# Optimization experiments

Measured on AMD Instinct MI355X. Metric: run time of the kernel, lower is better.

Reference implementation:

```python
import jax, jax.numpy as jnp
import numpy as np
from jax import lax

T, B, I, H = 512, 256, 128, 256

def setup_inputs() -> dict:
    key = jax.random.key(0)
    k1, k2, k3, k4 = jax.random.split(key, 4)
    x = jax.random.normal(k1, (T, B, I), dtype=jnp.float32)
    h0 = jnp.zeros((B, H), dtype=jnp.float32)
    Wi = jax.random.normal(k2, (H, I), dtype=jnp.float32) * (1.0 / np.sqrt(I))
    Wh = jax.random.normal(k3, (H, H), dtype=jnp.float32) * (1.0 / np.sqrt(H))
    bh = jax.random.normal(k4, (H,), dtype=jnp.float32) * 0.01
    return {"x": x, "h0": h0, "Wi": Wi, "Wh": Wh, "bh": bh}

def reference(x, h0, Wi, Wh, bh):
    # Precompute input projection for all timesteps: [T, B, H]
    xi = jnp.einsum("tbi,hi->tbh", x, Wi) + bh
    def step(h, xi_t):
        h_new = jnp.tanh(xi_t + h @ Wh.T)
        return h_new, h_new
    _, hs = lax.scan(step, h0, xi)
    return hs  # [T, B, H] hidden states, matching torch stack(out[1:])
```

## Files before the change

kernel.cpp:

```cpp
#include <hip/hip_runtime.h>
#include <hip/hip_bf16.h>
#include <math.h>

#define TT 512
#define BB 256
#define II 128
#define HH 256

#define TANH_S 2.885390043258667f


#define FCHUNK(CNT, A0,A1,B0,B1,C0,C1,D0,D1, H0,H1) \
        "s_waitcnt lgkmcnt(" CNT ")\n" \
        "v_pk_fma_f32 v[32:33], v[" A0 "], v[" H0 "], v[32:33]\n" \
        "v_pk_fma_f32 v[34:35], v[" B0 "], v[" H0 "], v[34:35]\n" \
        "v_pk_fma_f32 v[36:37], v[" C0 "], v[" H0 "], v[36:37]\n" \
        "v_pk_fma_f32 v[38:39], v[" D0 "], v[" H0 "], v[38:39]\n" \
        "v_pk_fma_f32 v[32:33], v[" A1 "], v[" H1 "], v[32:33]\n" \
        "v_pk_fma_f32 v[34:35], v[" B1 "], v[" H1 "], v[34:35]\n" \
        "v_pk_fma_f32 v[36:37], v[" C1 "], v[" H1 "], v[36:37]\n" \
        "v_pk_fma_f32 v[38:39], v[" D1 "], v[" H1 "], v[38:39]\n"

#define HSTORE \
        "global_store_dword v25, v30, %[iob]\n" \
        "v_add_u32 v25, 0x40000, v25\n"

#define FBODY(XNR, XCR, VC, ST) \
        ST \
         \
        "s_and_saveexec_b64 s[86:87], %[mskx]\n" \
        "global_load_dwordx4 " XNR ", v18, %[xb]\n" \
        "s_mov_b64 exec, s[86:87]\n" \
        "v_add_u32 v18, 0x20000, v18\n" \
        "v_min_u32 v18, %[vxomax], v18\n" \
         \
        "ds_read_b128 v[40:43], v16\n" \
        "ds_read_b128 v[44:47], v16 offset:16\n" \
        "ds_read_b128 v[48:51], v16 offset:32\n" \
        "ds_read_b128 v[52:55], v16 offset:48\n" \
        "ds_read_b128 v[56:59], v16 offset:64\n" \
        "ds_read_b128 v[60:63], v16 offset:80\n" \
        "s_setprio 1\n" \
         \
        "s_waitcnt lgkmcnt(5)\n" \
        "v_pk_mul_f32 v[32:33], v[64:65],   v[40:41]\n" \
        "v_pk_mul_f32 v[34:35], v[96:97],   v[40:41]\n" \
        "v_pk_mul_f32 v[36:37], v[128:129], v[40:41]\n" \
        "v_pk_mul_f32 v[38:39], v[160:161], v[40:41]\n" \
        "v_pk_fma_f32 v[32:33], v[66:67],   v[42:43], v[32:33]\n" \
        "v_pk_fma_f32 v[34:35], v[98:99],   v[42:43], v[34:35]\n" \
        "v_pk_fma_f32 v[36:37], v[130:131], v[42:43], v[36:37]\n" \
        "v_pk_fma_f32 v[38:39], v[162:163], v[42:43], v[38:39]\n" \
        "ds_read_b128 v[40:43], v16 offset:96\n" \
        FCHUNK("5","68:69","70:71","100:101","102:103","132:133","134:135","164:165","166:167","44:45","46:47") \
        "ds_read_b128 v[44:47], v16 offset:112\n" \
        FCHUNK("5","72:73","74:75","104:105","106:107","136:137","138:139","168:169","170:171","48:49","50:51") \
        "ds_read_b128 v[48:51], v16 offset:128\n" \
        FCHUNK("5","76:77","78:79","108:109","110:111","140:141","142:143","172:173","174:175","52:53","54:55") \
        "ds_read_b128 v[52:55], v16 offset:144\n" \
        FCHUNK("5","80:81","82:83","112:113","114:115","144:145","146:147","176:177","178:179","56:57","58:59") \
        "ds_read_b128 v[56:59], v16 offset:160\n" \
        FCHUNK("5","84:85","86:87","116:117","118:119","148:149","150:151","180:181","182:183","60:61","62:63") \
        "ds_read_b128 v[60:63], v16 offset:176\n" \
        FCHUNK("5","88:89","90:91","120:121","122:123","152:153","154:155","184:185","186:187","40:41","42:43") \
        FCHUNK("4","92:93","94:95","124:125","126:127","156:157","158:159","188:189","190:191","44:45","46:47") \
        FCHUNK("3","192:193","194:195","208:209","210:211","224:225","226:227","240:241","242:243","48:49","50:51") \
        FCHUNK("2","196:197","198:199","212:213","214:215","228:229","230:231","244:245","246:247","52:53","54:55") \
        FCHUNK("1","200:201","202:203","216:217","218:219","232:233","234:235","248:249","250:251","56:57","58:59") \
        FCHUNK("0","204:205","206:207","220:221","222:223","236:237","238:239","252:253","254:255","60:61","62:63") \
        "s_setprio 0\n" \
         \
        "s_waitcnt vmcnt(" VC ")\n" \
        "s_and_saveexec_b64 s[86:87], %[mskx]\n" \
        "ds_write_b128 v24, " XCR "\n" \
        "s_mov_b64 exec, s[86:87]\n" \
        "v_xor_b32 v24, 0x800, v24\n" \
         \
        "v_add_f32 v32, v32, v33\n" \
        "v_add_f32 v34, v34, v35\n" \
        "v_add_f32 v36, v36, v37\n" \
        "v_add_f32 v38, v38, v39\n" \
         \
        "v_add_f32 v32, v32, v32 quad_perm:[1,0,3,2] row_mask:0xf bank_mask:0xf\n" \
        "v_add_f32 v34, v34, v34 quad_perm:[1,0,3,2] row_mask:0xf bank_mask:0xf\n" \
        "v_add_f32 v36, v36, v36 quad_perm:[1,0,3,2] row_mask:0xf bank_mask:0xf\n" \
        "v_add_f32 v38, v38, v38 quad_perm:[1,0,3,2] row_mask:0xf bank_mask:0xf\n" \
        "v_add_f32 v32, v32, v32 quad_perm:[2,3,0,1] row_mask:0xf bank_mask:0xf\n" \
        "v_add_f32 v34, v34, v34 quad_perm:[2,3,0,1] row_mask:0xf bank_mask:0xf\n" \
        "v_add_f32 v36, v36, v36 quad_perm:[2,3,0,1] row_mask:0xf bank_mask:0xf\n" \
        "v_add_f32 v38, v38, v38 quad_perm:[2,3,0,1] row_mask:0xf bank_mask:0xf\n" \
         \
        "v_cndmask_b32 v30, v32, v34, %[m0]\n" \
        "v_cndmask_b32 v31, v36, v38, %[m0]\n" \
        "v_cndmask_b32 v30, v30, v31, %[m1]\n" \
         \
        "s_nop 1\n" \
        "v_add_f32 v30, v30, v30 row_ror:8 row_mask:0xf bank_mask:0xf\n" \
         \
        "v_add_f32 v30, v30, v19\n" \
        "v_exp_f32 v31, v30\n" \
        "s_nop 0\n" \
        "v_add_f32 v31, 1.0, v31\n" \
        "v_rcp_f32 v31, v31\n" \
        "s_nop 0\n" \
        "v_fma_f32 v30, -2.0, v31, 1.0\n" \
         \
        "s_and_saveexec_b64 s[84:85], %[msk]\n" \
        "ds_write_b32 v17, v30\n" \
        "s_mov_b64 exec, s[84:85]\n" \
        "v_xor_b32 v17, 0x800, v17\n" \
        "s_waitcnt lgkmcnt(0)\n" \
        "s_barrier\n" \
        "v_xor_b32 v16, 0x800, v16\n"

#define SCALE_PAIR(P) "v_pk_mul_f32 v[" P "], v[" P "], v[26:27]\n"

__global__ __launch_bounds__(512, 2) void rnn_fused_kernel(
    const float* __restrict__ x,  const float* __restrict__ h0,
    const float* __restrict__ Wi, const float* __restrict__ Wh,
    const float* __restrict__ bh, float* __restrict__ out)
{
    __shared__ float hbuf[928];

    const int tid  = threadIdx.x;
    const int b    = blockIdx.x;
    const int lane = tid & 63;
    const int q    = tid >> 6;
    const int kg   = (lane & 3) | ((lane >> 1) & 4);
    const int cg   = ((lane >> 2) & 1) | ((lane >> 3) & 6);
    const int col0 = 32 * q + 4 * cg;
    const int col  = col0 + (kg & 3);

    const float* wp  = Wh + (size_t)col0 * HH + kg * 32;
    const float* wip = Wi + (size_t)col0 * II + kg * 16;
    const float* iob = out + (size_t)b * HH;
    const float* xb  = x   + (size_t)b * II;
    unsigned hbase = (unsigned)(size_t)&hbuf[0];
    unsigned hvr = hbase + kg * 208;
    unsigned hvw = hbase + 0x800 + q * 208 + (4 * cg + (kg & 3)) * 4;
    unsigned vxw = hbase + 0x800 + (tid >> 2) * 208 + 128 + 16 * (tid & 3);
    unsigned vxo = (unsigned)(16 * tid) + 0x20000u;
    unsigned vxomax = (unsigned)(16 * tid) + 511u * 0x20000u;
    unsigned vho = (unsigned)(col * 4);
    float bhv = bh[col] * TANH_S;
    unsigned long long m0   = __ballot((lane & 1) != 0);
    unsigned long long m1   = __ballot((lane & 2) != 0);
    unsigned long long msk  = __ballot(kg < 4);
    unsigned long long mskx = __ballot(tid < 32);

    if (tid < HH) hbuf[(tid >> 5) * 52 + (tid & 31)] = h0[(size_t)b * HH + tid];
    if (tid < II) hbuf[(tid >> 4) * 52 + 32 + (tid & 15)] = xb[tid];
    __syncthreads();

    asm volatile(
        "global_load_dwordx4 v[64:67],   %[wp], off\n"
        "global_load_dwordx4 v[68:71],   %[wp], off offset:16\n"
        "global_load_dwordx4 v[72:75],   %[wp], off offset:32\n"
        "global_load_dwordx4 v[76:79],   %[wp], off offset:48\n"
        "global_load_dwordx4 v[80:83],   %[wp], off offset:64\n"
        "global_load_dwordx4 v[84:87],   %[wp], off offset:80\n"
        "global_load_dwordx4 v[88:91],   %[wp], off offset:96\n"
        "global_load_dwordx4 v[92:95],   %[wp], off offset:112\n"
        "global_load_dwordx4 v[96:99],   %[wp], off offset:1024\n"
        "global_load_dwordx4 v[100:103], %[wp], off offset:1040\n"
        "global_load_dwordx4 v[104:107], %[wp], off offset:1056\n"
        "global_load_dwordx4 v[108:111], %[wp], off offset:1072\n"
        "global_load_dwordx4 v[112:115], %[wp], off offset:1088\n"
        "global_load_dwordx4 v[116:119], %[wp], off offset:1104\n"
        "global_load_dwordx4 v[120:123], %[wp], off offset:1120\n"
        "global_load_dwordx4 v[124:127], %[wp], off offset:1136\n"
        "global_load_dwordx4 v[128:131], %[wp], off offset:2048\n"
        "global_load_dwordx4 v[132:135], %[wp], off offset:2064\n"
        "global_load_dwordx4 v[136:139], %[wp], off offset:2080\n"
        "global_load_dwordx4 v[140:143], %[wp], off offset:2096\n"
        "global_load_dwordx4 v[144:147], %[wp], off offset:2112\n"
        "global_load_dwordx4 v[148:151], %[wp], off offset:2128\n"
        "global_load_dwordx4 v[152:155], %[wp], off offset:2144\n"
        "global_load_dwordx4 v[156:159], %[wp], off offset:2160\n"
        "global_load_dwordx4 v[160:163], %[wp], off offset:3072\n"
        "global_load_dwordx4 v[164:167], %[wp], off offset:3088\n"
        "global_load_dwordx4 v[168:171], %[wp], off offset:3104\n"
        "global_load_dwordx4 v[172:175], %[wp], off offset:3120\n"
        "global_load_dwordx4 v[176:179], %[wp], off offset:3136\n"
        "global_load_dwordx4 v[180:183], %[wp], off offset:3152\n"
        "global_load_dwordx4 v[184:187], %[wp], off offset:3168\n"
        "global_load_dwordx4 v[188:191], %[wp], off offset:3184\n"
        "global_load_dwordx4 v[192:195], %[wip], off\n"
        "global_load_dwordx4 v[196:199], %[wip], off offset:16\n"
        "global_load_dwordx4 v[200:203], %[wip], off offset:32\n"
        "global_load_dwordx4 v[204:207], %[wip], off offset:48\n"
        "global_load_dwordx4 v[208:211], %[wip], off offset:512\n"
        "global_load_dwordx4 v[212:215], %[wip], off offset:528\n"
        "global_load_dwordx4 v[216:219], %[wip], off offset:544\n"
        "global_load_dwordx4 v[220:223], %[wip], off offset:560\n"
        "global_load_dwordx4 v[224:227], %[wip], off offset:1024\n"
        "global_load_dwordx4 v[228:231], %[wip], off offset:1040\n"
        "global_load_dwordx4 v[232:235], %[wip], off offset:1056\n"
        "global_load_dwordx4 v[236:239], %[wip], off offset:1072\n"
        "global_load_dwordx4 v[240:243], %[wip], off offset:1536\n"
        "global_load_dwordx4 v[244:247], %[wip], off offset:1552\n"
        "global_load_dwordx4 v[248:251], %[wip], off offset:1568\n"
        "global_load_dwordx4 v[252:255], %[wip], off offset:1584\n"
        "v_mov_b32 v16, %[hvr]\n"
        "v_mov_b32 v17, %[hvw]\n"
        "v_mov_b32 v18, %[vxo]\n"
        "v_mov_b32 v19, %[bhv]\n"
        "v_mov_b32 v24, %[vxw]\n"
        "v_mov_b32 v25, %[vho]\n"
        "s_waitcnt vmcnt(0)\n"
        "v_mov_b32 v26, 0x4038aa3b\n"
        "v_mov_b32 v27, 0x4038aa3b\n"
        SCALE_PAIR("64:65")   SCALE_PAIR("66:67")   SCALE_PAIR("68:69")   SCALE_PAIR("70:71")
        SCALE_PAIR("72:73")   SCALE_PAIR("74:75")   SCALE_PAIR("76:77")   SCALE_PAIR("78:79")
        SCALE_PAIR("80:81")   SCALE_PAIR("82:83")   SCALE_PAIR("84:85")   SCALE_PAIR("86:87")
        SCALE_PAIR("88:89")   SCALE_PAIR("90:91")   SCALE_PAIR("92:93")   SCALE_PAIR("94:95")
        SCALE_PAIR("96:97")   SCALE_PAIR("98:99")   SCALE_PAIR("100:101") SCALE_PAIR("102:103")
        SCALE_PAIR("104:105") SCALE_PAIR("106:107") SCALE_PAIR("108:109") SCALE_PAIR("110:111")
        SCALE_PAIR("112:113") SCALE_PAIR("114:115") SCALE_PAIR("116:117") SCALE_PAIR("118:119")
        SCALE_PAIR("120:121") SCALE_PAIR("122:123") SCALE_PAIR("124:125") SCALE_PAIR("126:127")
        SCALE_PAIR("128:129") SCALE_PAIR("130:131") SCALE_PAIR("132:133") SCALE_PAIR("134:135")
        SCALE_PAIR("136:137") SCALE_PAIR("138:139") SCALE_PAIR("140:141") SCALE_PAIR("142:143")
        SCALE_PAIR("144:145") SCALE_PAIR("146:147") SCALE_PAIR("148:149") SCALE_PAIR("150:151")
        SCALE_PAIR("152:153") SCALE_PAIR("154:155") SCALE_PAIR("156:157") SCALE_PAIR("158:159")
        SCALE_PAIR("160:161") SCALE_PAIR("162:163") SCALE_PAIR("164:165") SCALE_PAIR("166:167")
        SCALE_PAIR("168:169") SCALE_PAIR("170:171") SCALE_PAIR("172:173") SCALE_PAIR("174:175")
        SCALE_PAIR("176:177") SCALE_PAIR("178:179") SCALE_PAIR("180:181") SCALE_PAIR("182:183")
        SCALE_PAIR("184:185") SCALE_PAIR("186:187") SCALE_PAIR("188:189") SCALE_PAIR("190:191")
        SCALE_PAIR("192:193") SCALE_PAIR("194:195") SCALE_PAIR("196:197") SCALE_PAIR("198:199")
        SCALE_PAIR("200:201") SCALE_PAIR("202:203") SCALE_PAIR("204:205") SCALE_PAIR("206:207")
        SCALE_PAIR("208:209") SCALE_PAIR("210:211") SCALE_PAIR("212:213") SCALE_PAIR("214:215")
        SCALE_PAIR("216:217") SCALE_PAIR("218:219") SCALE_PAIR("220:221") SCALE_PAIR("222:223")
        SCALE_PAIR("224:225") SCALE_PAIR("226:227") SCALE_PAIR("228:229") SCALE_PAIR("230:231")
        SCALE_PAIR("232:233") SCALE_PAIR("234:235") SCALE_PAIR("236:237") SCALE_PAIR("238:239")
        SCALE_PAIR("240:241") SCALE_PAIR("242:243") SCALE_PAIR("244:245") SCALE_PAIR("246:247")
        SCALE_PAIR("248:249") SCALE_PAIR("250:251") SCALE_PAIR("252:253") SCALE_PAIR("254:255")
        "s_and_saveexec_b64 s[86:87], %[mskx]\n"
        "global_load_dwordx4 v[26:29], v18, %[xb]\n"
        "s_mov_b64 exec, s[86:87]\n"
        "v_add_u32 v18, 0x20000, v18\n"
        "s_movk_i32 s82, 0xFF\n"
        FBODY("v[20:23]", "v[26:29]", "1", "")
        FBODY("v[26:29]", "v[20:23]", "2", HSTORE)
        "LTOP_%=:\n"
        FBODY("v[20:23]", "v[26:29]", "2", HSTORE)
        FBODY("v[26:29]", "v[20:23]", "2", HSTORE)
        "s_sub_u32 s82, s82, 1\n"
        "s_cmp_lg_u32 s82, 0\n"
        "s_cbranch_scc1 LTOP_%=\n"
        "global_store_dword v25, v30, %[iob]\n"
        :
        : [wp] "v"(wp), [wip] "v"(wip), [iob] "s"(iob), [xb] "s"(xb),
          [hvr] "v"(hvr), [hvw] "v"(hvw), [vxo] "v"(vxo),
          [vxomax] "v"(vxomax), [vxw] "v"(vxw), [vho] "v"(vho),
          [bhv] "v"(bhv),
          [m0] "s"(m0), [m1] "s"(m1), [msk] "s"(msk), [mskx] "s"(mskx)
        : "memory", "scc", "s82", "s84", "s85", "s86", "s87",
          "v16","v17","v18","v19","v20","v21","v22","v23",
          "v24","v25","v26","v27","v28","v29","v30","v31",
          "v32","v33","v34","v35","v36","v37","v38","v39",
          "v40","v41","v42","v43","v44","v45","v46","v47",
          "v48","v49","v50","v51","v52","v53","v54","v55",
          "v56","v57","v58","v59","v60","v61","v62","v63",
          "v64","v65","v66","v67","v68","v69","v70","v71",
          "v72","v73","v74","v75","v76","v77","v78","v79",
          "v80","v81","v82","v83","v84","v85","v86","v87",
          "v88","v89","v90","v91","v92","v93","v94","v95",
          "v96","v97","v98","v99","v100","v101","v102","v103",
          "v104","v105","v106","v107","v108","v109","v110","v111",
          "v112","v113","v114","v115","v116","v117","v118","v119",
          "v120","v121","v122","v123","v124","v125","v126","v127",
          "v128","v129","v130","v131","v132","v133","v134","v135",
          "v136","v137","v138","v139","v140","v141","v142","v143",
          "v144","v145","v146","v147","v148","v149","v150","v151",
          "v152","v153","v154","v155","v156","v157","v158","v159",
          "v160","v161","v162","v163","v164","v165","v166","v167",
          "v168","v169","v170","v171","v172","v173","v174","v175",
          "v176","v177","v178","v179","v180","v181","v182","v183",
          "v184","v185","v186","v187","v188","v189","v190","v191",
          "v192","v193","v194","v195","v196","v197","v198","v199",
          "v200","v201","v202","v203","v204","v205","v206","v207",
          "v208","v209","v210","v211","v212","v213","v214","v215",
          "v216","v217","v218","v219","v220","v221","v222","v223",
          "v224","v225","v226","v227","v228","v229","v230","v231",
          "v232","v233","v234","v235","v236","v237","v238","v239",
          "v240","v241","v242","v243","v244","v245","v246","v247",
          "v248","v249","v250","v251","v252","v253","v254","v255");
}

extern "C" void kernel_launch(void* const* d_in, const int* in_sizes, int n_in,
                              void* d_out, int out_size, void* d_ws, size_t ws_size,
                              hipStream_t stream) {
    const float* x  = (const float*)d_in[0];
    const float* h0 = (const float*)d_in[1];
    const float* Wi = (const float*)d_in[2];
    const float* Wh = (const float*)d_in[3];
    const float* bh = (const float*)d_in[4];
    float* out = (float*)d_out;

    rnn_fused_kernel<<<BB, 512, 0, stream>>>(x, h0, Wi, Wh, bh, out);
}
```

Baseline: 326.1 us.

## Prefetch next-step x operands into registers before barrier to shorten the critical path

Each wave now loads its own slice of x (dwordx2 per lane) into a per-wave double-buffered LDS region instead of one masked 32-lane dwordx4 load. The x-part LDS reads for the next timestep are issued before the barrier, so the Wi*x FMAs can start at once without waiting on LDS. Only the h-part reads stay on the serial path. The h buffer stride shrinks and LDS use grows. The aim is to take the input-projection LDS latency off the per-step recurrent critical path.

```diff
diff --git a/kernel.cpp b/kernel.cpp
--- a/kernel.cpp
+++ b/kernel.cpp
@@ -21,60 +21,67 @@
         "v_pk_fma_f32 v[36:37], v[" C1 "], v[" H1 "], v[36:37]\n" \
         "v_pk_fma_f32 v[38:39], v[" D1 "], v[" H1 "], v[38:39]\n"
 
+#define FCHUNK_NW(A0,A1,B0,B1,C0,C1,D0,D1, H0,H1) \
+        "v_pk_fma_f32 v[32:33], v[" A0 "], v[" H0 "], v[32:33]\n" \
+        "v_pk_fma_f32 v[34:35], v[" B0 "], v[" H0 "], v[34:35]\n" \
+        "v_pk_fma_f32 v[36:37], v[" C0 "], v[" H0 "], v[36:37]\n" \
+        "v_pk_fma_f32 v[38:39], v[" D0 "], v[" H0 "], v[38:39]\n" \
+        "v_pk_fma_f32 v[32:33], v[" A1 "], v[" H1 "], v[32:33]\n" \
+        "v_pk_fma_f32 v[34:35], v[" B1 "], v[" H1 "], v[34:35]\n" \
+        "v_pk_fma_f32 v[36:37], v[" C1 "], v[" H1 "], v[36:37]\n" \
+        "v_pk_fma_f32 v[38:39], v[" D1 "], v[" H1 "], v[38:39]\n"
+
 #define HSTORE \
         "global_store_dword v25, v30, %[iob]\n" \
         "v_add_u32 v25, 0x40000, v25\n"
 
-#define FBODY(XNR, XCR, VC, ST) \
+#define FBODY(XN, XC, VC, ST) \
         ST \
          \
-        "s_and_saveexec_b64 s[86:87], %[mskx]\n" \
-        "global_load_dwordx4 " XNR ", v18, %[xb]\n" \
-        "s_mov_b64 exec, s[86:87]\n" \
+        "global_load_dwordx2 " XN ", v18, %[xb]\n" \
         "v_add_u32 v18, 0x20000, v18\n" \
         "v_min_u32 v18, %[vxomax], v18\n" \
          \
-        "ds_read_b128 v[40:43], v16\n" \
-        "ds_read_b128 v[44:47], v16 offset:16\n" \
-        "ds_read_b128 v[48:51], v16 offset:32\n" \
-        "ds_read_b128 v[52:55], v16 offset:48\n" \
-        "ds_read_b128 v[56:59], v16 offset:64\n" \
-        "ds_read_b128 v[60:63], v16 offset:80\n" \
+        "ds_read_b128 v[56:59], v16\n" \
+        "ds_read_b128 v[60:63], v16 offset:16\n" \
         "s_setprio 1\n" \
          \
-        "s_waitcnt lgkmcnt(5)\n" \
-        "v_pk_mul_f32 v[32:33], v[64:65],   v[40:41]\n" \
-        "v_pk_mul_f32 v[34:35], v[96:97],   v[40:41]\n" \
-        "v_pk_mul_f32 v[36:37], v[128:129], v[40:41]\n" \
-        "v_pk_mul_f32 v[38:39], v[160:161], v[40:41]\n" \
-        "v_pk_fma_f32 v[32:33], v[66:67],   v[42:43], v[32:33]\n" \
-        "v_pk_fma_f32 v[34:35], v[98:99],   v[42:43], v[34:35]\n" \
-        "v_pk_fma_f32 v[36:37], v[130:131], v[42:43], v[36:37]\n" \
-        "v_pk_fma_f32 v[38:39], v[162:163], v[42:43], v[38:39]\n" \
-        "ds_read_b128 v[40:43], v16 offset:96\n" \
-        FCHUNK("5","68:69","70:71","100:101","102:103","132:133","134:135","164:165","166:167","44:45","46:47") \
-        "ds_read_b128 v[44:47], v16 offset:112\n" \
-        FCHUNK("5","72:73","74:75","104:105","106:107","136:137","138:139","168:169","170:171","48:49","50:51") \
-        "ds_read_b128 v[48:51], v16 offset:128\n" \
-        FCHUNK("5","76:77","78:79","108:109","110:111","140:141","142:143","172:173","174:175","52:53","54:55") \
-        "ds_read_b128 v[52:55], v16 offset:144\n" \
-        FCHUNK("5","80:81","82:83","112:113","114:115","144:145","146:147","176:177","178:179","56:57","58:59") \
-        "ds_read_b128 v[56:59], v16 offset:160\n" \
-        FCHUNK("5","84:85","86:87","116:117","118:119","148:149","150:151","180:181","182:183","60:61","62:63") \
-        "ds_read_b128 v[60:63], v16 offset:176\n" \
-        FCHUNK("5","88:89","90:91","120:121","122:123","152:153","154:155","184:185","186:187","40:41","42:43") \
-        FCHUNK("4","92:93","94:95","124:125","126:127","156:157","158:159","188:189","190:191","44:45","46:47") \
-        FCHUNK("3","192:193","194:195","208:209","210:211","224:225","226:227","240:241","242:243","48:49","50:51") \
-        FCHUNK("2","196:197","198:199","212:213","214:215","228:229","230:231","244:245","246:247","52:53","54:55") \
-        FCHUNK("1","200:201","202:203","216:217","218:219","232:233","234:235","248:249","250:251","56:57","58:59") \
-        FCHUNK("0","204:205","206:207","220:221","222:223","236:237","238:239","252:253","254:255","60:61","62:63") \
+        "v_pk_mul_f32 v[32:33], v[192:193], v[40:41]\n" \
+        "v_pk_mul_f32 v[34:35], v[208:209], v[40:41]\n" \
+        "v_pk_mul_f32 v[36:37], v[224:225], v[40:41]\n" \
+        "v_pk_mul_f32 v[38:39], v[240:241], v[40:41]\n" \
+        "v_pk_fma_f32 v[32:33], v[194:195], v[42:43], v[32:33]\n" \
+        "v_pk_fma_f32 v[34:35], v[210:211], v[42:43], v[34:35]\n" \
+        "v_pk_fma_f32 v[36:37], v[226:227], v[42:43], v[36:37]\n" \
+        "v_pk_fma_f32 v[38:39], v[242:243], v[42:43], v[38:39]\n" \
+        "ds_read_b128 v[40:43], v16 offset:32\n"    \
+         \
+        FCHUNK_NW("196:197","198:199","212:213","214:215","228:229","230:231","244:245","246:247","44:45","46:47") \
+        "ds_read_b128 v[44:47], v16 offset:48\n"    \
+         \
+        FCHUNK_NW("200:201","202:203","216:217","218:219","232:233","234:235","248:249","250:251","48:49","50:51") \
+        "ds_read_b128 v[48:51], v16 offset:64\n"    \
+         \
+        FCHUNK_NW("204:205","206:207","220:221","222:223","236:237","238:239","252:253","254:255","52:53","54:55") \
+        "ds_read_b128 v[52:55], v16 offset:80\n"    \
+         \
+        FCHUNK("5","64:65","66:67","96:97","98:99","128:129","130:131","160:161","162:163","56:57","58:59") \
+        "ds_read_b128 v[56:59], v16 offset:96\n"    \
+         \
+        FCHUNK("5","68:69","70:71","100:101","102:103","132:133","134:135","164:165","166:167","60:61","62:63") \
+        "ds_read_b128 v[60:63], v16 offset:112\n"   \
+         \
+        FCHUNK("5","72:73","74:75","104:105","106:107","136:137","138:139","168:169","170:171","40:41","42:43") \
+        FCHUNK("4","76:77","78:79","108:109","110:111","140:141","142:143","172:173","174:175","44:45","46:47") \
+        FCHUNK("3","80:81","82:83","112:113","114:115","144:145","146:147","176:177","178:179","48:49","50:51") \
+        FCHUNK("2","84:85","86:87","116:117","118:119","148:149","150:151","180:181","182:183","52:53","54:55") \
+        FCHUNK("1","88:89","90:91","120:121","122:123","152:153","154:155","184:185","186:187","56:57","58:59") \
+        FCHUNK("0","92:93","94:95","124:125","126:127","156:157","158:159","188:189","190:191","60:61","62:63") \
         "s_setprio 0\n" \
          \
         "s_waitcnt vmcnt(" VC ")\n" \
-        "s_and_saveexec_b64 s[86:87], %[mskx]\n" \
-        "ds_write_b128 v24, " XCR "\n" \
-        "s_mov_b64 exec, s[86:87]\n" \
-        "v_xor_b32 v24, 0x800, v24\n" \
+        "ds_write_b64 v24, " XC "\n" \
+        "v_xor_b32 v24, 0x4000, v24\n" \
          \
         "v_add_f32 v32, v32, v33\n" \
         "v_add_f32 v34, v34, v35\n" \
@@ -109,6 +116,12 @@
         "ds_write_b32 v17, v30\n" \
         "s_mov_b64 exec, s[84:85]\n" \
         "v_xor_b32 v17, 0x800, v17\n" \
+         \
+        "ds_read_b128 v[40:43], v26\n" \
+        "ds_read_b128 v[44:47], v26 offset:16\n" \
+        "ds_read_b128 v[48:51], v26 offset:32\n" \
+        "ds_read_b128 v[52:55], v26 offset:48\n" \
+        "v_xor_b32 v26, 0x4000, v26\n" \
         "s_waitcnt lgkmcnt(0)\n" \
         "s_barrier\n" \
         "v_xor_b32 v16, 0x800, v16\n"
@@ -120,7 +133,7 @@
     const float* __restrict__ Wi, const float* __restrict__ Wh,
     const float* __restrict__ bh, float* __restrict__ out)
 {
-    __shared__ float hbuf[928];
+    __shared__ float hbuf[6400];
 
     const int tid  = threadIdx.x;
     const int b    = blockIdx.x;
@@ -136,20 +149,20 @@
     const float* iob = out + (size_t)b * HH;
     const float* xb  = x   + (size_t)b * II;
     unsigned hbase = (unsigned)(size_t)&hbuf[0];
-    unsigned hvr = hbase + kg * 208;
-    unsigned hvw = hbase + 0x800 + q * 208 + (4 * cg + (kg & 3)) * 4;
-    unsigned vxw = hbase + 0x800 + (tid >> 2) * 208 + 128 + 16 * (tid & 3);
-    unsigned vxo = (unsigned)(16 * tid) + 0x20000u;
-    unsigned vxomax = (unsigned)(16 * tid) + 511u * 0x20000u;
+    unsigned hvr = hbase + kg * 144;
+    unsigned hvw = hbase + 0x800 + q * 144 + (4 * cg + (kg & 3)) * 4;
+    unsigned xz  = hbase + 0x1000 + q * 640;
+    unsigned vxw = xz + ((lane >> 3) * 80) + ((lane & 7) * 8);
+    unsigned vxr = xz + kg * 80;
+    unsigned vxo = (unsigned)(lane * 8);
+    unsigned vxomax = vxo + 511u * 0x20000u;
     unsigned vho = (unsigned)(col * 4);
     float bhv = bh[col] * TANH_S;
-    unsigned long long m0   = __ballot((lane & 1) != 0);
-    unsigned long long m1   = __ballot((lane & 2) != 0);
-    unsigned long long msk  = __ballot(kg < 4);
-    unsigned long long mskx = __ballot(tid < 32);
-
-    if (tid < HH) hbuf[(tid >> 5) * 52 + (tid & 31)] = h0[(size_t)b * HH + tid];
-    if (tid < II) hbuf[(tid >> 4) * 52 + 32 + (tid & 15)] = xb[tid];
+    unsigned long long m0  = __ballot((lane & 1) != 0);
+    unsigned long long m1  = __ballot((lane & 2) != 0);
+    unsigned long long msk = __ballot(kg < 4);
+
+    if (tid < HH) hbuf[(tid >> 5) * 36 + (tid & 31)] = h0[(size_t)b * HH + tid];
     __syncthreads();
 
     asm volatile(
@@ -201,12 +214,6 @@
         "global_load_dwordx4 v[244:247], %[wip], off offset:1552\n"
         "global_load_dwordx4 v[248:251], %[wip], off offset:1568\n"
         "global_load_dwordx4 v[252:255], %[wip], off offset:1584\n"
-        "v_mov_b32 v16, %[hvr]\n"
-        "v_mov_b32 v17, %[hvw]\n"
-        "v_mov_b32 v18, %[vxo]\n"
-        "v_mov_b32 v19, %[bhv]\n"
-        "v_mov_b32 v24, %[vxw]\n"
-        "v_mov_b32 v25, %[vho]\n"
         "s_waitcnt vmcnt(0)\n"
         "v_mov_b32 v26, 0x4038aa3b\n"
         "v_mov_b32 v27, 0x4038aa3b\n"
@@ -234,16 +241,32 @@
         SCALE_PAIR("232:233") SCALE_PAIR("234:235") SCALE_PAIR("236:237") SCALE_PAIR("238:239")
         SCALE_PAIR("240:241") SCALE_PAIR("242:243") SCALE_PAIR("244:245") SCALE_PAIR("246:247")
         SCALE_PAIR("248:249") SCALE_PAIR("250:251") SCALE_PAIR("252:253") SCALE_PAIR("254:255")
-        "s_and_saveexec_b64 s[86:87], %[mskx]\n"
-        "global_load_dwordx4 v[26:29], v18, %[xb]\n"
-        "s_mov_b64 exec, s[86:87]\n"
+        "v_mov_b32 v16, %[hvr]\n"
+        "v_mov_b32 v17, %[hvw]\n"
+        "v_mov_b32 v18, %[vxo]\n"
+        "v_mov_b32 v19, %[bhv]\n"
+        "v_mov_b32 v24, %[vxw]\n"
+        "v_mov_b32 v25, %[vho]\n"
+        "v_mov_b32 v26, %[vxr]\n"
+        "global_load_dwordx2 v[20:21], v18, %[xb]\n"
         "v_add_u32 v18, 0x20000, v18\n"
+        "global_load_dwordx2 v[22:23], v18, %[xb]\n"
+        "v_add_u32 v18, 0x20000, v18\n"
+        "s_waitcnt vmcnt(1)\n"
+        "ds_write_b64 v24, v[20:21]\n"
+        "v_xor_b32 v24, 0x4000, v24\n"
+        "ds_read_b128 v[40:43], v26\n"
+        "ds_read_b128 v[44:47], v26 offset:16\n"
+        "ds_read_b128 v[48:51], v26 offset:32\n"
+        "ds_read_b128 v[52:55], v26 offset:48\n"
+        "v_xor_b32 v26, 0x4000, v26\n"
+        "s_waitcnt lgkmcnt(0)\n"
         "s_movk_i32 s82, 0xFF\n"
-        FBODY("v[20:23]", "v[26:29]", "1", "")
-        FBODY("v[26:29]", "v[20:23]", "2", HSTORE)
+        FBODY("v[20:21]", "v[22:23]", "1", "")
+        FBODY("v[22:23]", "v[20:21]", "2", HSTORE)
         "LTOP_%=:\n"
-        FBODY("v[20:23]", "v[26:29]", "2", HSTORE)
-        FBODY("v[26:29]", "v[20:23]", "2", HSTORE)
+        FBODY("v[20:21]", "v[22:23]", "2", HSTORE)
+        FBODY("v[22:23]", "v[20:21]", "2", HSTORE)
         "s_sub_u32 s82, s82, 1\n"
         "s_cmp_lg_u32 s82, 0\n"
         "s_cbranch_scc1 LTOP_%=\n"
@@ -251,10 +274,10 @@
         :
         : [wp] "v"(wp), [wip] "v"(wip), [iob] "s"(iob), [xb] "s"(xb),
           [hvr] "v"(hvr), [hvw] "v"(hvw), [vxo] "v"(vxo),
-          [vxomax] "v"(vxomax), [vxw] "v"(vxw), [vho] "v"(vho),
-          [bhv] "v"(bhv),
-          [m0] "s"(m0), [m1] "s"(m1), [msk] "s"(msk), [mskx] "s"(mskx)
-        : "memory", "scc", "s82", "s84", "s85", "s86", "s87",
+          [vxomax] "v"(vxomax), [vxw] "v"(vxw), [vxr] "v"(vxr),
+          [vho] "v"(vho), [bhv] "v"(bhv),
+          [m0] "s"(m0), [m1] "s"(m1), [msk] "s"(msk)
+        : "memory", "scc", "s82", "s84", "s85",
           "v16","v17","v18","v19","v20","v21","v22","v23",
           "v24","v25","v26","v27","v28","v29","v30","v31",
           "v32","v33","v34","v35","v36","v37","v38","v39",
```

After: 325.9 us. Within noise of the previous version (-0.0%).
